# Optimization experiments

Measured on AMD Instinct MI355X. Metric: run time of the kernel, lower is better.

The kernel has to match this reference:

```python
import jax, jax.numpy as jnp
import numpy as np

D, L, H = 10000, 512, 1024
B = 8

def setup_inputs() -> dict:
    key = jax.random.key(0)
    k1, k2, k3 = jax.random.split(key, 3)
    vocab = jax.random.normal(k1, (D, H), dtype=jnp.float32)
    description = jax.random.normal(k2, (B, L, H), dtype=jnp.float32)
    default_embedding = jax.random.uniform(k3, (H,), dtype=jnp.float32)
    return {"vocab": vocab, "description": description, "default_embedding": default_embedding}

def reference(vocab, description, default_embedding):
    # full_vocab: (D+1, H) -- concept vocab plus learned default embedding
    full_vocab = jnp.concatenate([vocab, default_embedding[None, :]], axis=0)
    # logits: (B, L, D+1) = tokens @ full_vocab.T (broadcast over batch, no repeat needed)
    logits = jnp.einsum('blh,dh->bld', description, full_vocab)
    similarity = jax.nn.softmax(logits, axis=2)
    # blend: default-slot weight times raw tokens + concept-weighted vocab mix
    concept_based = similarity[:, :, -1:] * description + jnp.einsum('bld,dh->blh', similarity[:, :, :-1], vocab)
    return (concept_based, similarity)
```

## Files before the change

### kernel.cpp

```cpp
#include <hip/hip_runtime.h>
#include <stdint.h>

#define D_    10000
#define DP1   10001
#define NPAD2 10240
#define LGW   10240
#define H_    1024
#define BL    4096
#define CANDS 1024
#define GC    512

typedef float  f32x4  __attribute__((ext_vector_type(4)));
typedef __bf16 bf16x8 __attribute__((ext_vector_type(8)));
typedef unsigned short u16;
typedef u16    u16x8  __attribute__((ext_vector_type(8)));

__device__ __forceinline__ u16 f2bf(float x) {
    union { float f; unsigned u; } v; v.f = x;
    unsigned r = v.u + 0x7FFFu + ((v.u >> 16) & 1u);
    return (u16)(r >> 16);
}
__device__ __forceinline__ float bf2f(u16 b) {
    union { float f; unsigned u; } v; v.u = ((unsigned)b) << 16;
    return v.f;
}

#define GLOAD_LDS16(gsrc, ldst)                                             \
    __builtin_amdgcn_global_load_lds(                                       \
        (__attribute__((address_space(1))) void*)(void*)(gsrc),             \
        (__attribute__((address_space(3))) void*)(void*)(ldst), 16, 0, 0)


__global__ __launch_bounds__(256)
void split_desc_k(const float* __restrict__ desc, u16* __restrict__ hi) {
    size_t i = ((size_t)blockIdx.x * 256 + threadIdx.x) * 8;
    f32x4 x0 = *(const f32x4*)(desc + i);
    f32x4 x1 = *(const f32x4*)(desc + i + 4);
    u16x8 h;
#pragma unroll
    for (int e = 0; e < 4; e++) { h[e] = f2bf(x0[e]); h[4 + e] = f2bf(x1[e]); }
    *(u16x8*)(hi + i) = h;
}

__global__ __launch_bounds__(256)
void split_fv_k(const float* __restrict__ vocab, const float* __restrict__ defe,
                u16* __restrict__ hi) {
    size_t i = ((size_t)blockIdx.x * 256 + threadIdx.x) * 8;
    int d = (int)(i >> 10);
    f32x4 x0 = {0.f, 0.f, 0.f, 0.f}, x1 = {0.f, 0.f, 0.f, 0.f};
    if (d < D_) {
        x0 = *(const f32x4*)(vocab + i);
        x1 = *(const f32x4*)(vocab + i + 4);
    } else if (d == D_) {
        int h = (int)(i & 1023);
        x0 = *(const f32x4*)(defe + h);
        x1 = *(const f32x4*)(defe + h + 4);
    }
    u16x8 h8;
#pragma unroll
    for (int e = 0; e < 4; e++) { h8[e] = f2bf(x0[e]); h8[4 + e] = f2bf(x1[e]); }
    *(u16x8*)(hi + i) = h8;
}


#define G1_MFMA(a, b, c) __builtin_amdgcn_mfma_f32_16x16x32_bf16((a), (b), (c), 0, 0, 0)

#define G1_STAGE(AhB, BhB, kk) do {                                         \
    GLOAD_LDS16(a_h  + (kk), (char*)(AhB) + tid16);                         \
    GLOAD_LDS16(b_h0 + (kk), (char*)(BhB) + tid16);                         \
    GLOAD_LDS16(b_h1 + (kk), (char*)(BhB) + tid16 + 8192);                  \
} while (0)

#define G1_ITER(AhB, BhB, t) do {                                           \
    bf16x8 afh[4], bfh[4];                                                  \
    _Pragma("unroll")                                                       \
    for (int i = 0; i < 4; i++) {                                           \
        afh[i] = *(const bf16x8*)&AhB[aoff[i]];                             \
        bfh[i] = *(const bf16x8*)&BhB[boff[i]];                             \
    }                                                                       \
    __builtin_amdgcn_s_setprio(1);                                          \
    _Pragma("unroll")                                                       \
    for (int i = 0; i < 2; i++)                                             \
        _Pragma("unroll")                                                   \
        for (int j = 0; j < 4; j++)                                         \
            acc[i][j] = G1_MFMA(afh[i], bfh[j], acc[i][j]);                 \
    __builtin_amdgcn_s_setprio(0);                                          \
    asm volatile("s_waitcnt lgkmcnt(0)" ::: "memory");                      \
    __builtin_amdgcn_s_barrier();                                           \
    if ((t) + 2 < 32) G1_STAGE(AhB, BhB, ((t) + 2) * 32);                   \
    __builtin_amdgcn_s_setprio(1);                                          \
    _Pragma("unroll")                                                       \
    for (int i = 2; i < 4; i++)                                             \
        _Pragma("unroll")                                                   \
        for (int j = 0; j < 4; j++)                                         \
            acc[i][j] = G1_MFMA(afh[i], bfh[j], acc[i][j]);                 \
    __builtin_amdgcn_s_setprio(0);                                          \
    if ((t) + 2 < 32)      asm volatile("s_waitcnt vmcnt(3)" ::: "memory"); \
    else if ((t) + 1 < 32) asm volatile("s_waitcnt vmcnt(0)" ::: "memory"); \
    __builtin_amdgcn_s_barrier();                                           \
} while (0)

__global__ __launch_bounds__(512, 2)
void gemm1_k(const u16* __restrict__ Ahg, const u16* __restrict__ Bhg,
             u16* __restrict__ Lg) {
    __shared__ u16 Ah0[128 * 32], Bh0[256 * 32];
    __shared__ u16 Ah1[128 * 32], Bh1[256 * 32];

    const int tid  = threadIdx.x;
    const int wave = tid >> 6, lane = tid & 63;
    const int wr = wave >> 2, wc = wave & 3;
    const int quad = lane >> 4, r16 = lane & 15;
    const int m0 = blockIdx.y * 128, n0 = blockIdx.x * 256;

    f32x4 zero = {0.f, 0.f, 0.f, 0.f};
    f32x4 acc[4][4];
#pragma unroll
    for (int i = 0; i < 4; i++)
#pragma unroll
        for (int j = 0; j < 4; j++) acc[i][j] = zero;

    const int arow = tid >> 2, achk = tid & 3;
    const int ascol = (achk ^ ((arow >> 1) & 3)) * 8;
    const u16* a_h = Ahg + (size_t)(m0 + arow) * H_ + ascol;
    const int brow0 = arow,        bscol0 = (achk ^ ((brow0 >> 1) & 3)) * 8;
    const int brow1 = 128 + arow,  bscol1 = (achk ^ ((brow1 >> 1) & 3)) * 8;
    const u16* b_h0 = Bhg + (size_t)(n0 + brow0) * H_ + bscol0;
    const u16* b_h1 = Bhg + (size_t)(n0 + brow1) * H_ + bscol1;
    const int tid16 = tid * 16;
    const int aswz = (r16 >> 1) & 3;

    int aoff[4], boff[4];
#pragma unroll
    for (int i = 0; i < 4; i++) {
        aoff[i] = (wr * 64 + i * 16 + r16) * 32 + ((quad ^ aswz) * 8);
        boff[i] = (wc * 64 + i * 16 + r16) * 32 + ((quad ^ aswz) * 8);
    }

    G1_STAGE(Ah0, Bh0, 0);
    G1_STAGE(Ah1, Bh1, 32);
    asm volatile("s_waitcnt vmcnt(3)" ::: "memory");
    __builtin_amdgcn_s_barrier();

    for (int t = 0; t < 32; t += 2) {
        G1_ITER(Ah0, Bh0, t);
        G1_ITER(Ah1, Bh1, t + 1);
    }

#pragma unroll
    for (int i = 0; i < 4; i++) {
        int gm = m0 + wr * 64 + i * 16 + quad * 4;
#pragma unroll
        for (int j = 0; j < 4; j++) {
            int gn = n0 + wc * 64 + j * 16 + r16;
#pragma unroll
            for (int reg = 0; reg < 4; reg++)
                Lg[(size_t)(gm + reg) * LGW + gn] = f2bf(acc[i][j][reg]);
        }
    }
}

__global__ __launch_bounds__(1024)
void softmax_finish_k(const u16* __restrict__ Lg, float* __restrict__ sim,
                      const float* __restrict__ vocab, const float* __restrict__ defe,
                      const float* __restrict__ desc, float* __restrict__ out) {
    __shared__ float red[16];
    __shared__ int   cnt;
    __shared__ int   cidx[GC];
    __shared__ float lex[GC + 1];
    __shared__ float psh[GC + 1];
    const int tid = threadIdx.x;
    const int row = blockIdx.x;
    const u16* lrow = Lg + (size_t)row * LGW;
    float* rowp = sim + (size_t)row * DP1;
    const float* drow = desc + (size_t)row * H_;
    if (tid == 0) cnt = 0;

    const int iA = tid * 8;
    const int iB = 8192 + tid * 8;
    float va[8], vb[8];
    {
        u16x8 ra = *(const u16x8*)(lrow + iA);
#pragma unroll
        for (int e = 0; e < 8; e++) va[e] = bf2f(ra[e]);
    }
    if (tid < 256) {
        u16x8 rb = *(const u16x8*)(lrow + iB);
#pragma unroll
        for (int e = 0; e < 8; e++) vb[e] = (iB + e <= D_) ? bf2f(rb[e]) : -3.4e38f;
    } else {
#pragma unroll
        for (int e = 0; e < 8; e++) vb[e] = -3.4e38f;
    }

    float mx = -3.4e38f;
#pragma unroll
    for (int e = 0; e < 8; e++) mx = fmaxf(mx, fmaxf(va[e], vb[e]));
#pragma unroll
    for (int off = 32; off; off >>= 1) mx = fmaxf(mx, __shfl_down(mx, off, 64));
    if ((tid & 63) == 0) red[tid >> 6] = mx;
    __syncthreads();
#pragma unroll
    for (int w = 0; w < 16; w++) mx = fmaxf(mx, red[w]);

    float s0 = 0.f;
#pragma unroll
    for (int e = 0; e < 8; e++) {
        va[e] = __expf(va[e] - mx); s0 += va[e];
        vb[e] = __expf(vb[e] - mx); s0 += vb[e];
    }
#pragma unroll
    for (int off = 32; off; off >>= 1) s0 += __shfl_down(s0, off, 64);
    __syncthreads();
    if ((tid & 63) == 0) red[tid >> 6] = s0;
    __syncthreads();
    float sum = 0.f;
#pragma unroll
    for (int w = 0; w < 16; w++) sum += red[w];
    const float inv = 1.f / sum;
    const float thr = sum * 1e-8f;

#pragma unroll
    for (int e = 0; e < 8; e++)
        if (va[e] > thr) {
            int k = atomicAdd(&cnt, 1);
            if (k < GC) cidx[k] = iA + e;
        }
    if (tid < 256) {
#pragma unroll
        for (int e = 0; e < 8; e++) {
            int idx = iB + e;
            if (idx < D_ && vb[e] > thr) {
                int k = atomicAdd(&cnt, 1);
                if (k < GC) cidx[k] = idx;
            }
        }
    }
    __syncthreads();

    const int cnt0 = cnt;
    const bool ovf = cnt0 > GC;
    const int cc = ovf ? GC : cnt0;
    const int lane = tid & 63, wv = tid >> 6;

    if (!ovf) {
        for (int c = wv; c <= cc; c += 16) {
            const float* vrow = (c == cc) ? defe : (vocab + (size_t)cidx[c] * H_);
            float s = 0.f;
#pragma unroll
            for (int q = 0; q < 4; q++) {
                f32x4 dv = *(const f32x4*)(drow + (q * 64 + lane) * 4);
                f32x4 vv = *(const f32x4*)(vrow + (q * 64 + lane) * 4);
                s += dv[0] * vv[0] + dv[1] * vv[1] + dv[2] * vv[2] + dv[3] * vv[3];
            }
#pragma unroll
            for (int off = 32; off; off >>= 1) s += __shfl_down(s, off, 64);
            if (lane == 0) lex[c] = s;
        }
        __syncthreads();
        float m = -3.4e38f;
        for (int c = 0; c <= cc; c++) m = fmaxf(m, lex[c]);
        float Z = 0.f;
        for (int c = 0; c <= cc; c++) Z += __expf(lex[c] - m);
        const float invZ = 1.f / Z;
        for (int i = tid; i <= cc; i += 1024) psh[i] = __expf(lex[i] - m) * invZ;
        __syncthreads();
    }

    {
        f32x4 p0, p1;
#pragma unroll
        for (int e = 0; e < 8; e++) {
            float p = va[e] * inv;
            if (!ovf && va[e] > thr) {
                for (int c = 0; c < cc; c++)
                    if (cidx[c] == iA + e) { p = psh[c]; break; }
            }
            if (e < 4) p0[e] = p; else p1[e - 4] = p;
        }
        *(f32x4*)(rowp + iA) = p0;
        *(f32x4*)(rowp + iA + 4) = p1;
    }
    if (tid < 256) {
#pragma unroll
        for (int e = 0; e < 8; e++) {
            int idx = iB + e;
            if (idx <= D_) {
                float p = vb[e] * inv;
                if (idx == D_) { if (!ovf) p = psh[cc]; }
                else if (!ovf && vb[e] > thr) {
                    for (int c = 0; c < cc; c++)
                        if (cidx[c] == idx) { p = psh[c]; break; }
                }
                rowp[idx] = p;
            }
        }
    }

    float a;
    if (!ovf) {
        a = psh[cc] * drow[tid];
        for (int c = 0; c < cc; c++)
            a += psh[c] * vocab[(size_t)cidx[c] * H_ + tid];
    } else {
        __syncthreads();
        a = rowp[D_] * drow[tid];
        for (int d = 0; d < D_; d++) {
            float p = rowp[d];
            if (p > 1e-8f) a += p * vocab[(size_t)d * H_ + tid];
        }
    }
    out[(size_t)row * H_ + tid] = a;
}

__global__ __launch_bounds__(256)
void naive_logits_k(const float* __restrict__ vocab, const float* __restrict__ desc,
                    const float* __restrict__ defe, float* __restrict__ sim) {
    int d = blockIdx.x * 256 + threadIdx.x;
    if (d >= DP1) return;
    const float* vr = (d < D_) ? (vocab + (size_t)d * H_) : defe;
    const float* dr = desc + (size_t)blockIdx.y * H_;
    float s = 0.f;
    for (int h = 0; h < H_; h++) s = fmaf(dr[h], vr[h], s);
    sim[(size_t)blockIdx.y * DP1 + d] = s;
}

__global__ __launch_bounds__(1024)
void softmax_gather_k(float* __restrict__ sim, const float* __restrict__ vocab,
                      const float* __restrict__ desc, float* __restrict__ out) {
    __shared__ float red[16];
    __shared__ float wslot;
    __shared__ int   cnt;
    __shared__ int   cidx[CANDS];
    __shared__ float cp[CANDS];
    const int tid = threadIdx.x;
    const int row = blockIdx.x;
    float* rowp = sim + (size_t)row * DP1;
    if (tid == 0) cnt = 0;

    const int a0 = (4 - (row & 3)) & 3;
    const int b0 = a0 + tid * 4;
    const int b1 = a0 + 4096 + tid * 4;
    const int b2 = a0 + 8192 + tid * 4;

    float vh = (tid < a0) ? rowp[tid] : -3.4e38f;
    f32x4 v0 = *(const f32x4*)(rowp + b0);
    f32x4 v1 = *(const f32x4*)(rowp + b1);
    f32x4 v2;
    if (b2 + 3 <= D_) {
        v2 = *(const f32x4*)(rowp + b2);
    } else {
#pragma unroll
        for (int e = 0; e < 4; e++)
            v2[e] = (b2 + e <= D_) ? rowp[b2 + e] : -3.4e38f;
    }

    float mx = vh;
#pragma unroll
    for (int e = 0; e < 4; e++) mx = fmaxf(mx, fmaxf(v0[e], fmaxf(v1[e], v2[e])));
#pragma unroll
    for (int off = 32; off; off >>= 1) mx = fmaxf(mx, __shfl_down(mx, off, 64));
    if ((tid & 63) == 0) red[tid >> 6] = mx;
    __syncthreads();
#pragma unroll
    for (int w = 0; w < 16; w++) mx = fmaxf(mx, red[w]);

    float s0 = 0.f;
    vh = __expf(vh - mx); s0 += vh;
#pragma unroll
    for (int e = 0; e < 4; e++) {
        v0[e] = __expf(v0[e] - mx); s0 += v0[e];
        v1[e] = __expf(v1[e] - mx); s0 += v1[e];
        v2[e] = __expf(v2[e] - mx); s0 += v2[e];
    }
#pragma unroll
    for (int off = 32; off; off >>= 1) s0 += __shfl_down(s0, off, 64);
    __syncthreads();
    if ((tid & 63) == 0) red[tid >> 6] = s0;
    __syncthreads();
    float sum = 0.f;
#pragma unroll
    for (int w = 0; w < 16; w++) sum += red[w];
    const float inv = 1.f / sum;
    const float thr = sum * 1e-7f;

    if (tid < a0) {
        float p = vh * inv;
        rowp[tid] = p;
        if (vh > thr) {
            int k = atomicAdd(&cnt, 1);
            if (k < CANDS) { cidx[k] = tid; cp[k] = p; }
        }
    }
    {
        f32x4 p0 = v0 * inv;
        *(f32x4*)(rowp + b0) = p0;
#pragma unroll
        for (int e = 0; e < 4; e++)
            if (v0[e] > thr) {
                int k = atomicAdd(&cnt, 1);
                if (k < CANDS) { cidx[k] = b0 + e; cp[k] = p0[e]; }
            }
        f32x4 p1 = v1 * inv;
        *(f32x4*)(rowp + b1) = p1;
#pragma unroll
        for (int e = 0; e < 4; e++)
            if (v1[e] > thr) {
                int k = atomicAdd(&cnt, 1);
                if (k < CANDS) { cidx[k] = b1 + e; cp[k] = p1[e]; }
            }
#pragma unroll
        for (int e = 0; e < 4; e++) {
            int idx = b2 + e;
            if (idx <= D_) {
                float p = v2[e] * inv;
                rowp[idx] = p;
                if (idx == D_) wslot = p;
                else if (v2[e] > thr) {
                    int k = atomicAdd(&cnt, 1);
                    if (k < CANDS) { cidx[k] = idx; cp[k] = p; }
                }
            }
        }
    }
    __syncthreads();

    const float w = wslot;
    float a = w * desc[(size_t)row * H_ + tid];
    if (cnt <= CANDS) {
        const int k = cnt;
        for (int c = 0; c < k; c++)
            a += cp[c] * vocab[(size_t)cidx[c] * H_ + tid];
    } else {
        const float pthr = thr * inv;
        for (int d = 0; d < D_; d++) {
            float p = rowp[d];
            if (p > pthr) a += p * vocab[(size_t)d * H_ + tid];
        }
    }
    out[(size_t)row * H_ + tid] = a;
}

extern "C" void kernel_launch(void* const* d_in, const int* in_sizes, int n_in,
                              void* d_out, int out_size, void* d_ws, size_t ws_size,
                              hipStream_t stream) {
    (void)in_sizes; (void)n_in; (void)out_size;
    const float* vocab = (const float*)d_in[0];
    const float* desc  = (const float*)d_in[1];
    const float* defe  = (const float*)d_in[2];
    float* out = (float*)d_out;
    float* sim = out + (size_t)BL * H_;

    const size_t REQ = 113246208ull;
    char* ws = (char*)d_ws;

    if (ws_size >= REQ) {
        u16* dhi = (u16*)(ws + 0);
        u16* fhi = (u16*)(ws + 8388608);
        u16* Lg  = (u16*)(ws + 29360128);

        split_desc_k<<<2048, 256, 0, stream>>>(desc, dhi);
        split_fv_k<<<5120, 256, 0, stream>>>(vocab, defe, fhi);
        gemm1_k<<<dim3(40, 32), 512, 0, stream>>>(dhi, fhi, Lg);
        softmax_finish_k<<<4096, 1024, 0, stream>>>(Lg, sim, vocab, defe, desc, out);
    } else {
        naive_logits_k<<<dim3(40, BL), 256, 0, stream>>>(vocab, desc, defe, sim);
        softmax_gather_k<<<4096, 1024, 0, stream>>>(sim, vocab, desc, out);
    }
}
```

Before: 434.3 us.

## Fuse partial softmax stats into GEMM epilogue and write fp32 logits in place

The GEMM epilogue now writes fp32 logits straight into the similarity output and computes per-64-column partial max and sum-of-exp per row into a small workspace. The finish kernel combines those partials into the row max and normalizer, then rewrites the logits in place as probabilities, replacing the bf16 logit scratch buffer and the block-wide reductions. The finish kernel also drops to 256 threads with float4 gathers. This trades a smaller intermediate for an extra fp32 read-modify-write of the 164 MB similarity tensor, and the partial stats come from bf16-product accumulators.

```diff
diff --git a/kernel.cpp b/kernel.cpp
--- a/kernel.cpp
+++ b/kernel.cpp
@@ -4,9 +4,9 @@
 #define D_    10000
 #define DP1   10001
 #define NPAD2 10240
-#define LGW   10240
 #define H_    1024
 #define BL    4096
+#define NPB   160
 #define CANDS 1024
 #define GC    512
 
@@ -19,10 +19,6 @@
     union { float f; unsigned u; } v; v.f = x;
     unsigned r = v.u + 0x7FFFu + ((v.u >> 16) & 1u);
     return (u16)(r >> 16);
-}
-__device__ __forceinline__ float bf2f(u16 b) {
-    union { float f; unsigned u; } v; v.u = ((unsigned)b) << 16;
-    return v.f;
 }
 
 #define GLOAD_LDS16(gsrc, ldst)                                             \
@@ -102,7 +98,7 @@
 
 __global__ __launch_bounds__(512, 2)
 void gemm1_k(const u16* __restrict__ Ahg, const u16* __restrict__ Bhg,
-             u16* __restrict__ Lg) {
+             float* __restrict__ C, float* __restrict__ Pt) {
     __shared__ u16 Ah0[128 * 32], Bh0[256 * 32];
     __shared__ u16 Ah1[128 * 32], Bh1[256 * 32];
 
@@ -152,86 +148,106 @@
 #pragma unroll
         for (int j = 0; j < 4; j++) {
             int gn = n0 + wc * 64 + j * 16 + r16;
-#pragma unroll
-            for (int reg = 0; reg < 4; reg++)
-                Lg[(size_t)(gm + reg) * LGW + gn] = f2bf(acc[i][j][reg]);
-        }
-    }
-}
-
-__global__ __launch_bounds__(1024)
-void softmax_finish_k(const u16* __restrict__ Lg, float* __restrict__ sim,
+            if (gn < DP1) {
+#pragma unroll
+                for (int reg = 0; reg < 4; reg++)
+                    C[(size_t)(gm + reg) * DP1 + gn] = acc[i][j][reg];
+            }
+        }
+    }
+    const int pcol = blockIdx.x * 4 + wc;
+#pragma unroll
+    for (int i = 0; i < 4; i++) {
+#pragma unroll
+        for (int reg = 0; reg < 4; reg++) {
+            float m = -3.4e38f;
+#pragma unroll
+            for (int j = 0; j < 4; j++) {
+                int gn = n0 + wc * 64 + j * 16 + r16;
+                if (gn < DP1) m = fmaxf(m, acc[i][j][reg]);
+            }
+#pragma unroll
+            for (int off = 1; off < 16; off <<= 1)
+                m = fmaxf(m, __shfl_xor(m, off, 64));
+            float s = 0.f;
+#pragma unroll
+            for (int j = 0; j < 4; j++) {
+                int gn = n0 + wc * 64 + j * 16 + r16;
+                if (gn < DP1) s += __expf(acc[i][j][reg] - m);
+            }
+#pragma unroll
+            for (int off = 1; off < 16; off <<= 1)
+                s += __shfl_xor(s, off, 64);
+            if (r16 == 0) {
+                int grow = m0 + wr * 64 + i * 16 + quad * 4 + reg;
+                float2 v; v.x = m; v.y = s;
+                *(float2*)(Pt + ((size_t)grow * NPB + pcol) * 2) = v;
+            }
+        }
+    }
+}
+
+__global__ __launch_bounds__(256)
+void softmax_finish_k(float* __restrict__ sim, const float* __restrict__ Pt,
                       const float* __restrict__ vocab, const float* __restrict__ defe,
                       const float* __restrict__ desc, float* __restrict__ out) {
-    __shared__ float red[16];
+    __shared__ float red[8];
     __shared__ int   cnt;
     __shared__ int   cidx[GC];
     __shared__ float lex[GC + 1];
     __shared__ float psh[GC + 1];
     const int tid = threadIdx.x;
     const int row = blockIdx.x;
-    const u16* lrow = Lg + (size_t)row * LGW;
     float* rowp = sim + (size_t)row * DP1;
     const float* drow = desc + (size_t)row * H_;
+    const int lane = tid & 63, wv = tid >> 6;
     if (tid == 0) cnt = 0;
 
-    const int iA = tid * 8;
-    const int iB = 8192 + tid * 8;
-    float va[8], vb[8];
+    float pm = -3.4e38f, ps = 0.f;
+    if (tid < NPB) {
+        float2 v = *(const float2*)(Pt + ((size_t)row * NPB + tid) * 2);
+        pm = v.x; ps = v.y;
+    }
+    float mt = pm;
+#pragma unroll
+    for (int off = 32; off; off >>= 1) mt = fmaxf(mt, __shfl_down(mt, off, 64));
+    if (lane == 0) red[wv] = mt;
+    __syncthreads();
+    const float M = fmaxf(fmaxf(red[0], red[1]), fmaxf(red[2], red[3]));
+    float zt = (tid < NPB) ? __expf(pm - M) * ps : 0.f;
+#pragma unroll
+    for (int off = 32; off; off >>= 1) zt += __shfl_down(zt, off, 64);
+    if (lane == 0) red[4 + wv] = zt;
+    __syncthreads();
+    const float Z = red[4] + red[5] + red[6] + red[7];
+    const float invZ = 1.f / Z;
+
+#pragma unroll
+    for (int s = 0; s < 9; s++) {
+        f32x4 l = *(const f32x4*)(rowp + s * 1024 + tid * 4);
+        f32x4 p;
+#pragma unroll
+        for (int e = 0; e < 4; e++) p[e] = __expf(l[e] - M) * invZ;
+        *(f32x4*)(rowp + s * 1024 + tid * 4) = p;
+#pragma unroll
+        for (int e = 0; e < 4; e++)
+            if (p[e] > 1e-8f) {
+                int k = atomicAdd(&cnt, 1);
+                if (k < GC) cidx[k] = s * 1024 + tid * 4 + e;
+            }
+    }
     {
-        u16x8 ra = *(const u16x8*)(lrow + iA);
-#pragma unroll
-        for (int e = 0; e < 8; e++) va[e] = bf2f(ra[e]);
-    }
-    if (tid < 256) {
-        u16x8 rb = *(const u16x8*)(lrow + iB);
-#pragma unroll
-        for (int e = 0; e < 8; e++) vb[e] = (iB + e <= D_) ? bf2f(rb[e]) : -3.4e38f;
-    } else {
-#pragma unroll
-        for (int e = 0; e < 8; e++) vb[e] = -3.4e38f;
-    }
-
-    float mx = -3.4e38f;
-#pragma unroll
-    for (int e = 0; e < 8; e++) mx = fmaxf(mx, fmaxf(va[e], vb[e]));
-#pragma unroll
-    for (int off = 32; off; off >>= 1) mx = fmaxf(mx, __shfl_down(mx, off, 64));
-    if ((tid & 63) == 0) red[tid >> 6] = mx;
-    __syncthreads();
-#pragma unroll
-    for (int w = 0; w < 16; w++) mx = fmaxf(mx, red[w]);
-
-    float s0 = 0.f;
-#pragma unroll
-    for (int e = 0; e < 8; e++) {
-        va[e] = __expf(va[e] - mx); s0 += va[e];
-        vb[e] = __expf(vb[e] - mx); s0 += vb[e];
-    }
-#pragma unroll
-    for (int off = 32; off; off >>= 1) s0 += __shfl_down(s0, off, 64);
-    __syncthreads();
-    if ((tid & 63) == 0) red[tid >> 6] = s0;
-    __syncthreads();
-    float sum = 0.f;
-#pragma unroll
-    for (int w = 0; w < 16; w++) sum += red[w];
-    const float inv = 1.f / sum;
-    const float thr = sum * 1e-8f;
-
-#pragma unroll
-    for (int e = 0; e < 8; e++)
-        if (va[e] > thr) {
-            int k = atomicAdd(&cnt, 1);
-            if (k < GC) cidx[k] = iA + e;
-        }
-    if (tid < 256) {
-#pragma unroll
-        for (int e = 0; e < 8; e++) {
-            int idx = iB + e;
-            if (idx < D_ && vb[e] > thr) {
-                int k = atomicAdd(&cnt, 1);
-                if (k < GC) cidx[k] = idx;
+        const int base = 9216 + tid * 4;
+#pragma unroll
+        for (int e = 0; e < 4; e++) {
+            int idx = base + e;
+            if (idx <= D_) {
+                float p = __expf(rowp[idx] - M) * invZ;
+                rowp[idx] = p;
+                if (idx < D_ && p > 1e-8f) {
+                    int k = atomicAdd(&cnt, 1);
+                    if (k < GC) cidx[k] = idx;
+                }
             }
         }
     }
@@ -240,10 +256,8 @@
     const int cnt0 = cnt;
     const bool ovf = cnt0 > GC;
     const int cc = ovf ? GC : cnt0;
-    const int lane = tid & 63, wv = tid >> 6;
-
     if (!ovf) {
-        for (int c = wv; c <= cc; c += 16) {
+        for (int c = wv; c <= cc; c += 4) {
             const float* vrow = (c == cc) ? defe : (vocab + (size_t)cidx[c] * H_);
             float s = 0.f;
 #pragma unroll
@@ -257,59 +271,28 @@
             if (lane == 0) lex[c] = s;
         }
         __syncthreads();
-        float m = -3.4e38f;
-        for (int c = 0; c <= cc; c++) m = fmaxf(m, lex[c]);
-        float Z = 0.f;
-        for (int c = 0; c <= cc; c++) Z += __expf(lex[c] - m);
-        const float invZ = 1.f / Z;
-        for (int i = tid; i <= cc; i += 1024) psh[i] = __expf(lex[i] - m) * invZ;
+        float m2 = -3.4e38f;
+        for (int c = 0; c <= cc; c++) m2 = fmaxf(m2, lex[c]);
+        float Z2 = 0.f;
+        for (int c = 0; c <= cc; c++) Z2 += __expf(lex[c] - m2);
+        const float iZ2 = 1.f / Z2;
+        for (int i = tid; i <= cc; i += 256) psh[i] = __expf(lex[i] - m2) * iZ2;
         __syncthreads();
-    }
-
-    {
-        f32x4 p0, p1;
-#pragma unroll
-        for (int e = 0; e < 8; e++) {
-            float p = va[e] * inv;
-            if (!ovf && va[e] > thr) {
-                for (int c = 0; c < cc; c++)
-                    if (cidx[c] == iA + e) { p = psh[c]; break; }
-            }
-            if (e < 4) p0[e] = p; else p1[e - 4] = p;
-        }
-        *(f32x4*)(rowp + iA) = p0;
-        *(f32x4*)(rowp + iA + 4) = p1;
-    }
-    if (tid < 256) {
-#pragma unroll
-        for (int e = 0; e < 8; e++) {
-            int idx = iB + e;
-            if (idx <= D_) {
-                float p = vb[e] * inv;
-                if (idx == D_) { if (!ovf) p = psh[cc]; }
-                else if (!ovf && vb[e] > thr) {
-                    for (int c = 0; c < cc; c++)
-                        if (cidx[c] == idx) { p = psh[c]; break; }
-                }
-                rowp[idx] = p;
-            }
-        }
-    }
-
-    float a;
-    if (!ovf) {
-        a = psh[cc] * drow[tid];
+        for (int c = tid; c < cc; c += 256) rowp[cidx[c]] = psh[c];
+        if (tid == 0) rowp[D_] = psh[cc];
+
+        f32x4 a = psh[cc] * ((const f32x4*)drow)[tid];
         for (int c = 0; c < cc; c++)
-            a += psh[c] * vocab[(size_t)cidx[c] * H_ + tid];
+            a += psh[c] * ((const f32x4*)(vocab + (size_t)cidx[c] * H_))[tid];
+        ((f32x4*)(out + (size_t)row * H_))[tid] = a;
     } else {
-        __syncthreads();
-        a = rowp[D_] * drow[tid];
+        f32x4 a = rowp[D_] * ((const f32x4*)drow)[tid];
         for (int d = 0; d < D_; d++) {
             float p = rowp[d];
-            if (p > 1e-8f) a += p * vocab[(size_t)d * H_ + tid];
-        }
-    }
-    out[(size_t)row * H_ + tid] = a;
+            if (p > 1e-8f) a += p * ((const f32x4*)(vocab + (size_t)d * H_))[tid];
+        }
+        ((f32x4*)(out + (size_t)row * H_))[tid] = a;
+    }
 }
 
 __global__ __launch_bounds__(256)
@@ -450,18 +433,18 @@
     float* out = (float*)d_out;
     float* sim = out + (size_t)BL * H_;
 
-    const size_t REQ = 113246208ull;
+    const size_t REQ = 34603008ull;
     char* ws = (char*)d_ws;
 
     if (ws_size >= REQ) {
-        u16* dhi = (u16*)(ws + 0);
-        u16* fhi = (u16*)(ws + 8388608);
-        u16* Lg  = (u16*)(ws + 29360128);
+        u16*   dhi = (u16*)(ws + 0);
+        u16*   fhi = (u16*)(ws + 8388608);
+        float* Pt  = (float*)(ws + 29360128);
 
         split_desc_k<<<2048, 256, 0, stream>>>(desc, dhi);
         split_fv_k<<<5120, 256, 0, stream>>>(vocab, defe, fhi);
-        gemm1_k<<<dim3(40, 32), 512, 0, stream>>>(dhi, fhi, Lg);
-        softmax_finish_k<<<4096, 1024, 0, stream>>>(Lg, sim, vocab, defe, desc, out);
+        gemm1_k<<<dim3(40, 32), 512, 0, stream>>>(dhi, fhi, sim, Pt);
+        softmax_finish_k<<<4096, 256, 0, stream>>>(sim, Pt, vocab, defe, desc, out);
     } else {
         naive_logits_k<<<dim3(40, BL), 256, 0, stream>>>(vocab, desc, defe, sim);
         softmax_gather_k<<<4096, 1024, 0, stream>>>(sim, vocab, desc, out);
```

New measurement: 410.6 us. -5.4%, faster.
